# Kernel optimization log

Measured on AMD Instinct MI355X. Metric: run time of the kernel, lower is better.

## Reference

```python
import jax, jax.numpy as jnp
import numpy as np

B, N, D, F_IN, F_OUT, MAX_DEG = 256, 512, 6, 128, 128, 6


def setup_inputs() -> dict:
    key = jax.random.key(0)
    k_atoms, k_deg, k_idx, k_w, k_b = jax.random.split(key, 5)
    atoms = jax.random.normal(k_atoms, (B, N, F_IN), dtype=jnp.float32)
    # structured edges: per-atom degree in [0, MAX_DEG-1], valid neighbor ids in
    # the first `deg` slots, -1 padding afterwards (NGFP convention)
    deg = jax.random.randint(k_deg, (B, N, 1), 0, MAX_DEG)
    nbr = jax.random.randint(k_idx, (B, N, D), 0, N)
    slot = jnp.arange(D)[None, None, :]
    edges = jnp.where(slot < deg, nbr, -1).astype(jnp.int64)
    W = jax.random.normal(k_w, (MAX_DEG, F_IN, F_OUT), dtype=jnp.float32) * (1.0 / np.sqrt(F_IN))
    b = jax.random.normal(k_b, (MAX_DEG, F_OUT), dtype=jnp.float32) * 0.01
    return {"atoms": atoms, "edges": edges, "W": W, "b": b}


def reference(atoms, edges, W, b):
    # lookup_neighbors with include_self=True: gather neighbor rows (-1 -> zero row)
    atoms_p = jnp.pad(atoms, ((0, 0), (1, 0), (0, 0)))          # [B, N+1, F]; row 0 is zeros
    gathered = jax.vmap(lambda a, e: a[e])(atoms_p, edges + 1)  # [B, N, D, F]
    summed = gathered.sum(axis=-2) + atoms                      # [B, N, F] (self included)
    degrees = (edges != -1).sum(axis=-1, keepdims=True)         # [B, N, 1]
    out = jnp.zeros(summed.shape[:-1] + (W.shape[-1],), dtype=summed.dtype)
    for d in range(MAX_DEG):
        h = jax.nn.relu(summed @ W[d] + b[d])                   # [B, N, F_OUT]
        out = out + h * (degrees == d).astype(summed.dtype)
    return out
```

## Files before the change

### kernel.cpp

```cpp
#include <hip/hip_runtime.h>


typedef short bf16x8 __attribute__((ext_vector_type(8)));
typedef float f32x4  __attribute__((ext_vector_type(4)));
typedef unsigned short ushort_t;
typedef unsigned int uint_t;

constexpr int Nn = 512;
constexpr int Ff = 128;

constexpr size_t WS_NEEDED = 196608;

__device__ inline ushort_t f2bf(float f) {
    uint_t u = __float_as_uint(f);
    return (ushort_t)((u + 0x7FFFu + ((u >> 16) & 1u)) >> 16);
}

__device__ inline bool detect_is64(const int* edges32) {
    int probe = edges32[2 * (threadIdx.x & 63) + 1];
    return __any(probe > 0) == 0;
}

__global__ __launch_bounds__(1024)
void k0_wt(const float* __restrict__ W, ushort_t* __restrict__ Wt) {
    int L = blockIdx.x * 1024 + threadIdx.x;
    int d = L >> 14, rem = L & 16383;
    int n = rem >> 7, k = rem & 127;
    Wt[L] = f2bf(W[(d << 14) + (k << 7) + n]);
}

__global__ __launch_bounds__(512, 2)
void k_fused(const float* __restrict__ atoms,
             const int*   __restrict__ edges32,
             const ushort_t* __restrict__ Wt,
             const float* __restrict__ bias,
             float* __restrict__ out) {
    const int tid = threadIdx.x;
    const int mol = blockIdx.x;
    const bool is64 = detect_is64(edges32);

    __shared__ ushort_t summed[Nn * 136];
    __shared__ float4   scratch4[1088];
    __shared__ ushort_t rlist[Nn];
    __shared__ int hist[6], base_sh[8];

    float4*   abuf4 = scratch4;
    ushort_t* Wsh   = (ushort_t*)scratch4;

    const float4* gsrc = (const float4*)(atoms + (size_t)mol * (Nn * Ff));
    float4 pf0 = gsrc[(tid >> 1) * 32 + (tid & 1)];
    float4 pf1 = gsrc[((tid + 512) >> 1) * 32 + (tid & 1)];

    int e_[6];
    {
        const size_t eb = (size_t)mol * (Nn * 6) + (size_t)tid * 6;
        #pragma unroll
        for (int j = 0; j < 6; j++)
            e_[j] = is64 ? edges32[(eb + j) * 2] : edges32[eb + j];
    }
    int deg = 0;
    #pragma unroll
    for (int j = 0; j < 6; j++) deg += (e_[j] >= 0) ? 1 : 0;
    if (deg > 5) deg = 5;
    int er[6];
    #pragma unroll
    for (int j = 0; j < 6; j++) er[j] = (e_[j] >= 0) ? e_[j] : Nn;

    if (tid < 6) hist[tid] = 0;
    if (tid < 2) abuf4[2 * Nn + tid] = make_float4(0.f, 0.f, 0.f, 0.f);
    __syncthreads();
    int rk = atomicAdd(&hist[deg], 1);
    __syncthreads();
    if (tid == 0) {
        int acc = 0;
        #pragma unroll
        for (int d = 0; d < 6; d++) { base_sh[d] = acc; acc += hist[d]; }
    }
    __syncthreads();
    rlist[base_sh[deg] + rk] = (ushort_t)tid;

    {
        int r0 = tid >> 1, c0 = tid & 1;
        abuf4[2 * r0 + (c0 ^ ((r0 >> 2) & 1))] = pf0;
        int r1 = (tid + 512) >> 1;
        abuf4[2 * r1 + (c0 ^ ((r1 >> 2) & 1))] = pf1;
    }
    __syncthreads();

    const int sg = (tid >> 2) & 1;
    for (int s = 0; s < 16; s++) {
        if (s < 15) {
            pf0 = gsrc[(tid >> 1) * 32 + (s + 1) * 2 + (tid & 1)];
            pf1 = gsrc[((tid + 512) >> 1) * 32 + (s + 1) * 2 + (tid & 1)];
        }
        float4 a0 = abuf4[2 * tid + sg];
        float4 a1 = abuf4[2 * tid + (1 ^ sg)];
        #pragma unroll
        for (int j = 0; j < 6; j++) {
            int e = er[j];
            int se = (e >> 2) & 1;
            float4 v0 = abuf4[2 * e + se];
            float4 v1 = abuf4[2 * e + (1 ^ se)];
            a0.x += v0.x; a0.y += v0.y; a0.z += v0.z; a0.w += v0.w;
            a1.x += v1.x; a1.y += v1.y; a1.z += v1.z; a1.w += v1.w;
        }
        uint4 o;
        o.x = (uint_t)f2bf(a0.x) | ((uint_t)f2bf(a0.y) << 16);
        o.y = (uint_t)f2bf(a0.z) | ((uint_t)f2bf(a0.w) << 16);
        o.z = (uint_t)f2bf(a1.x) | ((uint_t)f2bf(a1.y) << 16);
        o.w = (uint_t)f2bf(a1.z) | ((uint_t)f2bf(a1.w) << 16);
        *(uint4*)&summed[tid * 136 + s * 8] = o;
        __syncthreads();
        if (s < 15) {
            int r0 = tid >> 1, c0 = tid & 1;
            abuf4[2 * r0 + (c0 ^ ((r0 >> 2) & 1))] = pf0;
            int r1 = (tid + 512) >> 1;
            abuf4[2 * r1 + (c0 ^ ((r1 >> 2) & 1))] = pf1;
            __syncthreads();
        }
    }

    const int lane = tid & 63, wid = tid >> 6;
    const int kq = lane >> 4, ml = lane & 15;

    for (int d = 0; d < 6; d++) {
        const int cb = base_sh[d], cn = hist[d];
        const int Td = (cn + 15) >> 4;
        const uint4* wg = (const uint4*)(Wt + (size_t)d * 16384);
        for (int half = 0; half < 2; half++) {
            {
                int i0 = tid;
                int n = i0 >> 4, c = i0 & 15;
                *(uint4*)&Wsh[n * 136 + c * 8] = wg[half * 1024 + i0];
                int i1 = tid + 512;
                n = i1 >> 4; c = i1 & 15;
                *(uint4*)&Wsh[n * 136 + c * 8] = wg[half * 1024 + i1];
            }
            __syncthreads();
            const int items = Td * 2;
            for (int it = wid; it < items; it += 8) {
                const int ti = it >> 1, nh = it & 1;
                int lidx = ti * 16 + ml;
                int cl = (lidx < cn) ? lidx : cn - 1;
                int row = rlist[cb + cl];
                bf16x8 af[4];
                #pragma unroll
                for (int k0 = 0; k0 < 4; k0++)
                    af[k0] = *(const bf16x8*)&summed[row * 136 + kq * 8 + k0 * 32];
                int orw[4];
                #pragma unroll
                for (int r = 0; r < 4; r++) {
                    int li = ti * 16 + kq * 4 + r;
                    orw[r] = (li < cn) ? (int)rlist[cb + li] : -1;
                }
                #pragma unroll
                for (int n2 = 0; n2 < 2; n2++) {
                    const int nt = nh * 2 + n2;
                    bf16x8 bfr[4];
                    #pragma unroll
                    for (int k0 = 0; k0 < 4; k0++)
                        bfr[k0] = *(const bf16x8*)&Wsh[(nt * 16 + ml) * 136 + k0 * 32 + kq * 8];
                    f32x4 c = {0.f, 0.f, 0.f, 0.f};
                    #pragma unroll
                    for (int k0 = 0; k0 < 4; k0++)
                        c = __builtin_amdgcn_mfma_f32_16x16x32_bf16(af[k0], bfr[k0], c, 0, 0, 0);
                    const int col = half * 64 + nt * 16 + ml;
                    const float bc = bias[d * Ff + col];
                    #pragma unroll
                    for (int r = 0; r < 4; r++) {
                        if (orw[r] >= 0) {
                            float v = c[r] + bc;
                            out[((size_t)mol * Nn + orw[r]) * Ff + col] = v > 0.f ? v : 0.f;
                        }
                    }
                }
            }
            __syncthreads();
        }
    }
}

__global__ __launch_bounds__(128, 2)
void graphconv_fallback(const float* __restrict__ atoms,
                        const int* __restrict__ edges_raw,
                        const float* __restrict__ W,
                        const float* __restrict__ bias,
                        float* __restrict__ out) {
    const int tid = threadIdx.x;
    const int d = blockIdx.x % 6;
    const int k = blockIdx.x / 6;
    const int a0 = k * 256;
    __shared__ int eds[256 * 6];
    __shared__ int list[256];
    __shared__ int cnt;
    __shared__ float sv[2][Ff];
    bool is64;
    { int v = edges_raw[2 * (tid & 63) + 1]; is64 = (__ballot(v > 0) == 0ull); }
    if (!is64) { for (int i = tid; i < 256 * 6; i += 128) eds[i] = edges_raw[a0 * 6 + i]; }
    else       { for (int i = tid; i < 256 * 6; i += 128) eds[i] = edges_raw[2 * (a0 * 6 + i)]; }
    if (tid == 0) cnt = 0;
    __syncthreads();
    for (int i = tid; i < 256; i += 128) {
        int deg = 0;
        #pragma unroll
        for (int j = 0; j < 6; j++) deg += (eds[i * 6 + j] != -1) ? 1 : 0;
        if (deg == d) { int p = atomicAdd(&cnt, 1); list[p] = i; }
    }
    float Wreg[Ff];
    { const float* Wd = W + (size_t)d * Ff * Ff;
      #pragma unroll
      for (int f = 0; f < Ff; f++) Wreg[f] = Wd[f * Ff + tid]; }
    const float breg = bias[d * Ff + tid];
    __syncthreads();
    const int n = cnt;
    const float* batch_atoms = atoms + (size_t)(a0 / Nn) * Nn * Ff;
    const int row0 = a0 % Nn;
    for (int ii = 0; ii < n; ii++) {
        const int i = list[ii];
        float s = batch_atoms[(row0 + i) * Ff + tid];
        #pragma unroll
        for (int j = 0; j < 6; j++) {
            int e = eds[i * 6 + j];
            if (e != -1) s += batch_atoms[e * Ff + tid];
        }
        float* buf = sv[ii & 1];
        buf[tid] = s;
        __syncthreads();
        float acc = breg;
        const float4* sv4 = (const float4*)buf;
        #pragma unroll
        for (int fc = 0; fc < Ff / 4; fc++) {
            float4 x = sv4[fc];
            acc = fmaf(x.x, Wreg[4 * fc + 0], acc);
            acc = fmaf(x.y, Wreg[4 * fc + 1], acc);
            acc = fmaf(x.z, Wreg[4 * fc + 2], acc);
            acc = fmaf(x.w, Wreg[4 * fc + 3], acc);
        }
        out[(size_t)(a0 + i) * Ff + tid] = fmaxf(acc, 0.0f);
    }
}

extern "C" void kernel_launch(void* const* d_in, const int* in_sizes, int n_in,
                              void* d_out, int out_size, void* d_ws, size_t ws_size,
                              hipStream_t stream) {
    const float* atoms = (const float*)d_in[0];
    const int*   edges = (const int*)d_in[1];
    const float* W     = (const float*)d_in[2];
    const float* bias  = (const float*)d_in[3];
    float*       outp  = (float*)d_out;

    if (ws_size >= WS_NEEDED) {
        ushort_t* Wt = (ushort_t*)d_ws;
        k0_wt<<<96, 1024, 0, stream>>>(W, Wt);
        k_fused<<<256, 512, 0, stream>>>(atoms, edges, Wt, bias, outp);
    } else {
        graphconv_fallback<<<3072, 128, 0, stream>>>(atoms, edges, W, bias, outp);
    }
}
```

Measured before the change: 156.4 us.

## Use 1024 threads, degree-sorted gather, and flatten GEMM items reading weights from global

The fused kernel now runs 1024 threads per block. Each thread pair handles one atom row, taken in degree-sorted order, and neighbor accumulation skips padding edges instead of reading a zero row. The per-degree, per-half shared-memory weight staging and its barriers are removed: all degree tiles form one flat work list, and B fragments are read straight from the bf16 weight buffer in global/L2. This trades LDS weight reuse for fewer barriers and better load balance. The launch bound of (1024,4) may force register limits, and the larger LDS footprint may lower occupancy.

```diff
diff --git a/kernel.cpp b/kernel.cpp
--- a/kernel.cpp
+++ b/kernel.cpp
@@ -29,7 +29,7 @@
     Wt[L] = f2bf(W[(d << 14) + (k << 7) + n]);
 }
 
-__global__ __launch_bounds__(512, 2)
+__global__ __launch_bounds__(1024, 4)
 void k_fused(const float* __restrict__ atoms,
              const int*   __restrict__ edges32,
              const ushort_t* __restrict__ Wt,
@@ -40,82 +40,66 @@
     const bool is64 = detect_is64(edges32);
 
     __shared__ ushort_t summed[Nn * 136];
-    __shared__ float4   scratch4[1088];
+    __shared__ float4   abuf4[Nn * 2];
     __shared__ ushort_t rlist[Nn];
     __shared__ int hist[6], base_sh[8];
 
-    float4*   abuf4 = scratch4;
-    ushort_t* Wsh   = (ushort_t*)scratch4;
-
     const float4* gsrc = (const float4*)(atoms + (size_t)mol * (Nn * Ff));
-    float4 pf0 = gsrc[(tid >> 1) * 32 + (tid & 1)];
-    float4 pf1 = gsrc[((tid + 512) >> 1) * 32 + (tid & 1)];
-
-    int e_[6];
+    const int arow = tid >> 1, ac = tid & 1;
+    float4 pf = gsrc[arow * 32 + ac];
+
+    if (tid < 6) hist[tid] = 0;
+    __syncthreads();
+    int deg = 0, rk = 0;
+    if (tid < Nn) {
+        const size_t eb = (size_t)mol * (Nn * 6) + (size_t)tid * 6;
+        #pragma unroll
+        for (int j = 0; j < 6; j++) {
+            int e = is64 ? edges32[(eb + j) * 2] : edges32[eb + j];
+            deg += (e >= 0) ? 1 : 0;
+        }
+        if (deg > 5) deg = 5;
+        rk = atomicAdd(&hist[deg], 1);
+    }
+    __syncthreads();
+    if (tid == 0) {
+        int a = 0;
+        #pragma unroll
+        for (int d = 0; d < 6; d++) { base_sh[d] = a; a += hist[d]; }
+    }
+    __syncthreads();
+    if (tid < Nn) rlist[base_sh[deg] + rk] = (ushort_t)tid;
+    abuf4[2 * arow + (ac ^ (arow & 1))] = pf;
+    __syncthreads();
+
+    const int pr = tid >> 1, h = tid & 1;
+    const int R = rlist[pr];
+    int er[6];
     {
-        const size_t eb = (size_t)mol * (Nn * 6) + (size_t)tid * 6;
+        const size_t eb = (size_t)mol * (Nn * 6) + (size_t)R * 6;
         #pragma unroll
         for (int j = 0; j < 6; j++)
-            e_[j] = is64 ? edges32[(eb + j) * 2] : edges32[eb + j];
-    }
-    int deg = 0;
-    #pragma unroll
-    for (int j = 0; j < 6; j++) deg += (e_[j] >= 0) ? 1 : 0;
-    if (deg > 5) deg = 5;
-    int er[6];
-    #pragma unroll
-    for (int j = 0; j < 6; j++) er[j] = (e_[j] >= 0) ? e_[j] : Nn;
-
-    if (tid < 6) hist[tid] = 0;
-    if (tid < 2) abuf4[2 * Nn + tid] = make_float4(0.f, 0.f, 0.f, 0.f);
-    __syncthreads();
-    int rk = atomicAdd(&hist[deg], 1);
-    __syncthreads();
-    if (tid == 0) {
-        int acc = 0;
-        #pragma unroll
-        for (int d = 0; d < 6; d++) { base_sh[d] = acc; acc += hist[d]; }
-    }
-    __syncthreads();
-    rlist[base_sh[deg] + rk] = (ushort_t)tid;
-
-    {
-        int r0 = tid >> 1, c0 = tid & 1;
-        abuf4[2 * r0 + (c0 ^ ((r0 >> 2) & 1))] = pf0;
-        int r1 = (tid + 512) >> 1;
-        abuf4[2 * r1 + (c0 ^ ((r1 >> 2) & 1))] = pf1;
-    }
-    __syncthreads();
-
-    const int sg = (tid >> 2) & 1;
+            er[j] = is64 ? edges32[(eb + j) * 2] : edges32[eb + j];
+    }
+
     for (int s = 0; s < 16; s++) {
-        if (s < 15) {
-            pf0 = gsrc[(tid >> 1) * 32 + (s + 1) * 2 + (tid & 1)];
-            pf1 = gsrc[((tid + 512) >> 1) * 32 + (s + 1) * 2 + (tid & 1)];
-        }
-        float4 a0 = abuf4[2 * tid + sg];
-        float4 a1 = abuf4[2 * tid + (1 ^ sg)];
+        if (s < 15) pf = gsrc[arow * 32 + (s + 1) * 2 + ac];
+        float4 a = abuf4[2 * R + (h ^ (R & 1))];
         #pragma unroll
         for (int j = 0; j < 6; j++) {
             int e = er[j];
-            int se = (e >> 2) & 1;
-            float4 v0 = abuf4[2 * e + se];
-            float4 v1 = abuf4[2 * e + (1 ^ se)];
-            a0.x += v0.x; a0.y += v0.y; a0.z += v0.z; a0.w += v0.w;
-            a1.x += v1.x; a1.y += v1.y; a1.z += v1.z; a1.w += v1.w;
-        }
-        uint4 o;
-        o.x = (uint_t)f2bf(a0.x) | ((uint_t)f2bf(a0.y) << 16);
-        o.y = (uint_t)f2bf(a0.z) | ((uint_t)f2bf(a0.w) << 16);
-        o.z = (uint_t)f2bf(a1.x) | ((uint_t)f2bf(a1.y) << 16);
-        o.w = (uint_t)f2bf(a1.z) | ((uint_t)f2bf(a1.w) << 16);
-        *(uint4*)&summed[tid * 136 + s * 8] = o;
+            if (e >= 0) {
+                float4 v = abuf4[2 * e + (h ^ (e & 1))];
+                a.x += v.x; a.y += v.y; a.z += v.z; a.w += v.w;
+            }
+        }
+        uint2 o;
+        o.x = (uint_t)f2bf(a.x) | ((uint_t)f2bf(a.y) << 16);
+        o.y = (uint_t)f2bf(a.z) | ((uint_t)f2bf(a.w) << 16);
+        *(uint2*)&summed[R * 136 + s * 8 + h * 4] = o;
         __syncthreads();
         if (s < 15) {
-            int r0 = tid >> 1, c0 = tid & 1;
-            abuf4[2 * r0 + (c0 ^ ((r0 >> 2) & 1))] = pf0;
-            int r1 = (tid + 512) >> 1;
-            abuf4[2 * r1 + (c0 ^ ((r1 >> 2) & 1))] = pf1;
+            abuf4[2 * arow + (ac ^ (arow & 1))] = pf;
             __syncthreads();
         }
     }
@@ -123,59 +107,61 @@
     const int lane = tid & 63, wid = tid >> 6;
     const int kq = lane >> 4, ml = lane & 15;
 
-    for (int d = 0; d < 6; d++) {
-        const int cb = base_sh[d], cn = hist[d];
-        const int Td = (cn + 15) >> 4;
-        const uint4* wg = (const uint4*)(Wt + (size_t)d * 16384);
-        for (int half = 0; half < 2; half++) {
-            {
-                int i0 = tid;
-                int n = i0 >> 4, c = i0 & 15;
-                *(uint4*)&Wsh[n * 136 + c * 8] = wg[half * 1024 + i0];
-                int i1 = tid + 512;
-                n = i1 >> 4; c = i1 & 15;
-                *(uint4*)&Wsh[n * 136 + c * 8] = wg[half * 1024 + i1];
-            }
-            __syncthreads();
-            const int items = Td * 2;
-            for (int it = wid; it < items; it += 8) {
-                const int ti = it >> 1, nh = it & 1;
-                int lidx = ti * 16 + ml;
-                int cl = (lidx < cn) ? lidx : cn - 1;
-                int row = rlist[cb + cl];
-                bf16x8 af[4];
-                #pragma unroll
-                for (int k0 = 0; k0 < 4; k0++)
-                    af[k0] = *(const bf16x8*)&summed[row * 136 + kq * 8 + k0 * 32];
-                int orw[4];
-                #pragma unroll
-                for (int r = 0; r < 4; r++) {
-                    int li = ti * 16 + kq * 4 + r;
-                    orw[r] = (li < cn) ? (int)rlist[cb + li] : -1;
-                }
-                #pragma unroll
-                for (int n2 = 0; n2 < 2; n2++) {
-                    const int nt = nh * 2 + n2;
-                    bf16x8 bfr[4];
-                    #pragma unroll
-                    for (int k0 = 0; k0 < 4; k0++)
-                        bfr[k0] = *(const bf16x8*)&Wsh[(nt * 16 + ml) * 136 + k0 * 32 + kq * 8];
-                    f32x4 c = {0.f, 0.f, 0.f, 0.f};
-                    #pragma unroll
-                    for (int k0 = 0; k0 < 4; k0++)
-                        c = __builtin_amdgcn_mfma_f32_16x16x32_bf16(af[k0], bfr[k0], c, 0, 0, 0);
-                    const int col = half * 64 + nt * 16 + ml;
-                    const float bc = bias[d * Ff + col];
-                    #pragma unroll
-                    for (int r = 0; r < 4; r++) {
-                        if (orw[r] >= 0) {
-                            float v = c[r] + bc;
-                            out[((size_t)mol * Nn + orw[r]) * Ff + col] = v > 0.f ? v : 0.f;
-                        }
-                    }
+    int cnts[6], cbase[6], Tp[7];
+    {
+        int a = 0, b = 0;
+        #pragma unroll
+        for (int d = 0; d < 6; d++) {
+            cnts[d] = hist[d];
+            cbase[d] = b; b += cnts[d];
+            Tp[d] = a; a += ((cnts[d] + 15) >> 4) * 4;
+        }
+        Tp[6] = a;
+    }
+    const int items = Tp[6];
+
+    for (int it = wid; it < items; it += 16) {
+        int d = 0;
+        #pragma unroll
+        for (int dd = 1; dd < 6; dd++) if (it >= Tp[dd]) d = dd;
+        const int loc = it - Tp[d];
+        const int ti = loc >> 2, ci = loc & 3;
+        const int cn = cnts[d], cb = cbase[d];
+
+        int lidx = ti * 16 + ml;
+        int cl = (lidx < cn) ? lidx : cn - 1;
+        int row = rlist[cb + cl];
+        bf16x8 af[4];
+        #pragma unroll
+        for (int k0 = 0; k0 < 4; k0++)
+            af[k0] = *(const bf16x8*)&summed[row * 136 + kq * 8 + k0 * 32];
+        int orw[4];
+        #pragma unroll
+        for (int r = 0; r < 4; r++) {
+            int li = ti * 16 + kq * 4 + r;
+            orw[r] = (li < cn) ? (int)rlist[cb + li] : -1;
+        }
+        const ushort_t* wg = Wt + (size_t)d * 16384;
+        #pragma unroll
+        for (int n2 = 0; n2 < 2; n2++) {
+            const int nt = ci * 2 + n2;
+            bf16x8 bfr[4];
+            #pragma unroll
+            for (int k0 = 0; k0 < 4; k0++)
+                bfr[k0] = *(const bf16x8*)&wg[(nt * 16 + ml) * 128 + k0 * 32 + kq * 8];
+            f32x4 c = {0.f, 0.f, 0.f, 0.f};
+            #pragma unroll
+            for (int k0 = 0; k0 < 4; k0++)
+                c = __builtin_amdgcn_mfma_f32_16x16x32_bf16(af[k0], bfr[k0], c, 0, 0, 0);
+            const int col = nt * 16 + ml;
+            const float bc = bias[d * Ff + col];
+            #pragma unroll
+            for (int r = 0; r < 4; r++) {
+                if (orw[r] >= 0) {
+                    float v = c[r] + bc;
+                    out[((size_t)mol * Nn + orw[r]) * Ff + col] = v > 0.f ? v : 0.f;
                 }
             }
-            __syncthreads();
         }
     }
 }
@@ -252,7 +238,7 @@
     if (ws_size >= WS_NEEDED) {
         ushort_t* Wt = (ushort_t*)d_ws;
         k0_wt<<<96, 1024, 0, stream>>>(W, Wt);
-        k_fused<<<256, 512, 0, stream>>>(atoms, edges, Wt, bias, outp);
+        k_fused<<<256, 1024, 0, stream>>>(atoms, edges, Wt, bias, outp);
     } else {
         graphconv_fallback<<<3072, 128, 0, stream>>>(atoms, edges, W, bias, outp);
     }
```

Result: no change. 157.3 us (+0.5%).
